# Kernel tuning notes

Measured on AMD Instinct MI355X. Metric: run time of the kernel, lower is better.

The kernel has to match this reference:

```python
import jax, jax.numpy as jnp
import numpy as np
import math
from jax import lax

# cfg['MODEL'] constants
MU = 0.1          # FISTA step size
LMBD = 0.1        # LAMBDA[0], sparsity weight
N_DICT = 1        # EXPANSION_FACTOR
N_STEPS = 6       # NUM_LAYERS (FISTA iterations)
K = 3             # kernel_size
PAD = 1           # padding
STRIDE = 1        # stride (POOLING=False, stride passed to conv)
DN = ('NCHW', 'OIHW', 'NCHW')


def _conv(x, w):
    # F.conv2d(x, w, stride=1, padding=PAD)
    return lax.conv_general_dilated(x, w, (STRIDE, STRIDE), [(PAD, PAD), (PAD, PAD)], dimension_numbers=DN)


def _conv_t(y, w):
    # F.conv_transpose2d(y, w, stride=1, padding=PAD) == conv2d with flipped, in/out-swapped kernel, pad K-1-PAD
    wt = jnp.transpose(jnp.flip(w, (-1, -2)), (1, 0, 2, 3))  # [Cin, Cout, K, K]
    p = K - 1 - PAD
    return lax.conv_general_dilated(y, wt, (1, 1), [(p, p), (p, p)], dimension_numbers=DN)


def _shrink(z, thr):
    # non_negative=True soft-threshold: relu(z - thr)
    return jax.nn.relu(z - thr)


def setup_inputs() -> dict:
    key = jax.random.key(0)
    k1, k2 = jax.random.split(key)
    x = jax.random.normal(k1, (16, 64, 56, 56), dtype=jnp.float32)
    # dictionary weight [out_channels, in_channels*n_dict, K, K], kaiming-ish scale
    W = jax.random.normal(k2, (128, 64 * N_DICT, K, K), dtype=jnp.float32) * 0.05
    return {"x": x, "W": W}


def reference(x, W):
    # w_norm: each output filter normalized to unit Frobenius norm
    Wn = W / jnp.sqrt(jnp.sum(W * W, axis=(1, 2, 3), keepdims=True) + 1e-12)
    thr = MU * LMBD
    xr = jnp.tile(x, (1, N_DICT, 1, 1)) if N_DICT > 1 else x

    # FISTA iteration 0: c = shrink(mu * D^T x)
    c = _shrink(MU * _conv(xr, Wn), thr)
    y = c
    c_prev = c
    t = 1.0
    for _ in range(N_STEPS - 1):
        r = xr - _conv_t(y, Wn)                       # residual x - D c
        c_new = _shrink(y + MU * _conv(r, Wn), thr)   # gradient step + shrink
        t_next = (1.0 + math.sqrt(1.0 + 4.0 * t * t)) / 2.0
        y = c_new + ((t - 1.0) / t_next) * (c_new - c_prev)  # momentum
        c_prev = c_new
        t = t_next
    # POOLING=False -> DictConv2d returns the sparse code directly
    return c_prev
```

## Files before the change

### kernel.cpp

```cpp
#include <hip/hip_runtime.h>
#include <hip/hip_bf16.h>
#include <math.h>

typedef __attribute__((ext_vector_type(8))) short short8;
typedef __attribute__((ext_vector_type(4))) float f32x4;

#define MU_  0.1f
#define THR_ 0.01f
#define ZB_  204

static __device__ inline short f2bf(float f) {
    __hip_bfloat16 h = __float2bfloat16(f);
    return *reinterpret_cast<short*>(&h);
}
static __device__ inline float bf2f(unsigned short u) {
    unsigned int x = ((unsigned int)u) << 16;
    return __builtin_bit_cast(float, x);
}

__global__ __launch_bounds__(256) void prep_kernel(
    const float* __restrict__ x, const float* __restrict__ W,
    short* __restrict__ Rp, short* __restrict__ Yp,
    short* __restrict__ Xp, short* __restrict__ Wf2, short* __restrict__ Wt2) {
    __shared__ float lx[64 * 57];
    const int bid = blockIdx.x, tid = threadIdx.x;
    if (bid < ZB_) {
        int gid = bid * 256 + tid;
        const short8 z = {0, 0, 0, 0, 0, 0, 0, 0};
        if (gid < 17408) {
            int ridx = gid / 544, off = gid - ridx * 544;
            int n = ridx >> 1, row = (ridx & 1) * 57;
            ((short8*)(Rp + ((size_t)(n * 58 + row) * 68) * 64))[off] = z;
        } else {
            int g2 = gid - 17408;
            int ridx = g2 / 1088, off = g2 - ridx * 1088;
            int n = ridx >> 1, row = (ridx & 1) * 57;
            ((short8*)(Yp + ((size_t)(n * 58 + row) * 68) * 128))[off] = z;
        }
    } else if (bid < ZB_ + 32) {
        int co = (bid - ZB_) * 4 + (tid >> 6);
        int ci = tid & 63;
        const float* wp = W + (co * 64 + ci) * 9;
        float v[9]; float s = 0.f;
#pragma unroll
        for (int t = 0; t < 9; ++t) { v[t] = wp[t]; s += v[t] * v[t]; }
#pragma unroll
        for (int off = 32; off; off >>= 1) s += __shfl_xor(s, off, 64);
        float inv = 1.0f / sqrtf(s + 1e-12f);
#pragma unroll
        for (int t = 0; t < 9; ++t) {
            Wf2[((t * 8 + (ci >> 3)) * 128 + co) * 8 + (ci & 7)] = f2bf(v[t] * inv);
            Wt2[((t * 16 + (co >> 3)) * 64 + ci) * 8 + (co & 7)] = f2bf(v[8 - t] * inv);
        }
    } else {
        int pb = bid - ZB_ - 32;
        int row = pb % 58, n = pb / 58;
        short* dst = Xp + ((size_t)(n * 58 + row) * 68) * 64;
        if (row >= 1 && row <= 56) {
            int h = row - 1;
            for (int j = tid; j < 64 * 56; j += 256) {
                int ci = j / 56, w = j - ci * 56;
                lx[ci * 57 + w] = x[((size_t)(n * 64 + ci)) * 3136 + h * 56 + w];
            }
            __syncthreads();
            for (int j = tid; j < 68 * 64; j += 256) {
                int s = j >> 6, ci = j & 63;
                float val = (s >= 2 && s < 58) ? lx[ci * 57 + (s - 2)] : 0.f;
                dst[(s << 6) + (ci ^ ((s & 7) << 3))] = f2bf(val);
            }
        } else {
            for (int j = tid; j < 68 * 64; j += 256) dst[j] = 0;
        }
    }
}

static __device__ __forceinline__ void zero_lds_pads(short* smem, int tid) {
    const short8 z = {0, 0, 0, 0, 0, 0, 0, 0};
    for (int i = tid; i < 288; i += 256) {
        int sr = i >> 3, w = i & 7;
        int row = sr / 12, sl = sr - row * 12;
        int s = (sl < 2) ? sl : sl + 56;
        *(short8*)(smem + (row * 68 + s) * 72 + w * 8) = z;
    }
}

__global__ __launch_bounds__(256, 4) void conv_fwd(
    const short* __restrict__ inp,
    const short* __restrict__ Wf2,
    short* __restrict__ Yp,
    short* __restrict__ Cp,
    float* __restrict__ outp, int mode, float beta) {
    __shared__ __align__(16) short smem[14688];
    const int bid = blockIdx.x, tid = threadIdx.x;
    const int sid = (bid & 7) * 112 + (bid >> 3);
    const int n = sid / 56, r = sid - n * 56 + 1;
    zero_lds_pads(smem, tid);
    {
        const short8* src = (const short8*)(inp + ((size_t)(n * 58 + (r - 1)) * 68) * 64);
        for (int j = tid; j < 1344; j += 256) {
            int sr = j >> 3, w = j & 7;
            int row = sr / 56, s = sr - row * 56 + 2;
            *(short8*)(smem + (row * 68 + s) * 72 + w * 8) = src[(row * 68 + s) * 8 + w];
        }
    }
    const int lane = tid & 63, ct = tid >> 6, quad = lane >> 4, l15 = lane & 15;
    const int cog = ct & 1, pxg = ct >> 1;
    const size_t prow = ((size_t)(n * 58 + r) * 68) * 128;

    short8 yold8[2], cold8[2];
    int pvv[2], pg[2]; bool pok[2];
#pragma unroll
    for (int k = 0; k < 2; ++k) {
        int item = tid + k * 256;
        pok[k] = item < 448;
        pvv[k] = item >> 3; pg[k] = item & 7;
        if (mode != 0 && pok[k]) {
            int s = pvv[k] + 2;
            size_t off = prow + (size_t)s * 128 + 8 * (pg[k] ^ (s & 7));
            yold8[k] = *(const short8*)(Yp + off);
            if (mode == 1) cold8[k] = *(const short8*)(Cp + off);
        }
    }
    __syncthreads();

    f32x4 acc[2][4];
#pragma unroll
    for (int pt = 0; pt < 2; ++pt)
#pragma unroll
        for (int cot = 0; cot < 4; ++cot) acc[pt][cot] = (f32x4){0.f, 0.f, 0.f, 0.f};

#pragma unroll
    for (int f = 0; f < 18; ++f) {
        const int t = f >> 1, half = f & 1;
        const int dh = t / 3, dw = t % 3;
        const int u = l15 + dw + 1;
        const int phys = (half * 4 + quad) ^ (u & 7);
        short8 areg[4];
#pragma unroll
        for (int cot = 0; cot < 4; ++cot) {
            const int co = cog * 64 + cot * 16 + l15;
            areg[cot] = *(const short8*)(Wf2 +
                ((size_t)((t * 8 + half * 4 + quad) * 128 + co)) * 8);
        }
#pragma unroll
        for (int pt = 0; pt < 2; ++pt) {
            const int pti = pxg * 2 + pt;
            const short8 bv = *(const short8*)(smem +
                (dh * 68 + pti * 16 + u) * 72 + phys * 8);
#pragma unroll
            for (int cot = 0; cot < 4; ++cot)
                acc[pt][cot] = __builtin_amdgcn_mfma_f32_16x16x32_bf16(areg[cot], bv, acc[pt][cot], 0, 0, 0);
        }
    }

    __syncthreads();
    short* tb_y = smem;
    short* tb_c = smem + 4608;
    const int h = r - 1;
#pragma unroll
    for (int hh = 0; hh < 2; ++hh) {
        if (mode != 0) {
#pragma unroll
            for (int k = 0; k < 2; ++k) if (pok[k]) {
                int o = pvv[k] * 72 + 8 * (pg[k] ^ (pvv[k] & 3));
                *(short8*)(tb_y + o) = yold8[k];
                if (mode == 1) *(short8*)(tb_c + o) = cold8[k];
            }
        }
        __syncthreads();
        if (hh == 0 && mode != 0) {
#pragma unroll
            for (int k = 0; k < 2; ++k) if (pok[k]) {
                int s = pvv[k] + 2;
                size_t off = prow + (size_t)s * 128 + 8 * ((pg[k] + 8) ^ (s & 7));
                yold8[k] = *(const short8*)(Yp + off);
                if (mode == 1) cold8[k] = *(const short8*)(Cp + off);
            }
        }
        if (cog == hh) {
#pragma unroll
            for (int pt = 0; pt < 2; ++pt) {
                const int px = pxg * 32 + pt * 16 + l15;
#pragma unroll
                for (int cot = 0; cot < 4; ++cot) {
#pragma unroll
                    for (int reg = 0; reg < 4; ++reg) {
                        const int lch = cot * 16 + quad * 4 + reg;
                        const int slot = px * 72 + (lch ^ ((px & 3) << 3));
                        const float a = acc[pt][cot][reg];
                        if (mode == 0) {
                            float c = fmaxf(MU_ * a - THR_, 0.f);
                            short cb16 = f2bf(c);
                            tb_y[slot] = cb16;
                            tb_c[slot] = cb16;
                        } else if (mode == 1) {
                            float yold = bf2f((unsigned short)tb_y[slot]);
                            float cold = bf2f((unsigned short)tb_c[slot]);
                            float c = fmaxf(yold + MU_ * a - THR_, 0.f);
                            tb_y[slot] = f2bf(c + beta * (c - cold));
                            tb_c[slot] = f2bf(c);
                        } else {
                            if (px < 56) {
                                float yold = bf2f((unsigned short)tb_y[slot]);
                                float c = fmaxf(yold + MU_ * a - THR_, 0.f);
                                outp[((size_t)(n * 128 + hh * 64 + lch)) * 3136 + h * 56 + px] = c;
                            }
                        }
                    }
                }
            }
        }
        if (mode != 2) {
            __syncthreads();
            for (int item = tid; item < 448; item += 256) {
                int vv = item >> 3, g = item & 7;
                int so = vv * 72 + 8 * (g ^ (vv & 3));
                short8 yv = *(const short8*)(tb_y + so);
                short8 cv = *(const short8*)(tb_c + so);
                int s = vv + 2;
                size_t off = prow + (size_t)s * 128 + 8 * ((g + 8 * hh) ^ (s & 7));
                *(short8*)(Yp + off) = yv;
                *(short8*)(Cp + off) = cv;
            }
        }
        if (hh == 0) __syncthreads();
    }
}

__global__ __launch_bounds__(256, 4) void conv_t(
    const short* __restrict__ Ypb,
    const short* __restrict__ Wt2,
    const short* __restrict__ Xp,
    short* __restrict__ Rp) {
    __shared__ __align__(16) short smem[14688];
    const int bid = blockIdx.x, tid = threadIdx.x;
    const int sid = (bid & 7) * 112 + (bid >> 3);
    const int n = sid / 56, r = sid - n * 56 + 1;
    const int lane = tid & 63, ct = tid >> 6, quad = lane >> 4, l15 = lane & 15;
    const short8* src = (const short8*)(Ypb + ((size_t)(n * 58 + (r - 1)) * 68) * 128);
    const size_t prow = ((size_t)(n * 58 + r) * 68) * 64;

    short8 xold8[2];
    int pvv[2], pg[2]; bool pok[2];
#pragma unroll
    for (int k = 0; k < 2; ++k) {
        int item = tid + k * 256;
        pok[k] = item < 448;
        pvv[k] = item >> 3; pg[k] = item & 7;
        if (pok[k]) {
            int s = pvv[k] + 2;
            xold8[k] = *(const short8*)(Xp + prow + (size_t)s * 64 + 8 * (pg[k] ^ (s & 7)));
        }
    }

    zero_lds_pads(smem, tid);
    for (int j = tid; j < 1344; j += 256) {
        int sr = j >> 3, w = j & 7;
        int row = sr / 56, s = sr - row * 56 + 2;
        *(short8*)(smem + (row * 68 + s) * 72 + w * 8) = src[(row * 68 + s) * 16 + w];
    }

    f32x4 acc[4];
#pragma unroll
    for (int cit = 0; cit < 4; ++cit) acc[cit] = (f32x4){0.f, 0.f, 0.f, 0.f};

    __syncthreads();

    short8 pf[6];
#pragma unroll
    for (int k = 0; k < 6; ++k) {
        int j = tid + k * 256;
        if (j < 1344) {
            int sr = j >> 3, w = j & 7;
            int row = sr / 56, s = sr - row * 56 + 2;
            pf[k] = src[(row * 68 + s) * 16 + 8 + w];
        }
    }

#pragma unroll
    for (int p = 0; p < 2; ++p) {
        if (p) {
            __syncthreads();
#pragma unroll
            for (int k = 0; k < 6; ++k) {
                int j = tid + k * 256;
                if (j < 1344) {
                    int sr = j >> 3, w = j & 7;
                    int row = sr / 56, s = sr - row * 56 + 2;
                    *(short8*)(smem + (row * 68 + s) * 72 + w * 8) = pf[k];
                }
            }
            __syncthreads();
        }
#pragma unroll
        for (int f = 0; f < 18; ++f) {
            const int t = f >> 1, sh = f & 1;
            const int dh = t / 3, dw = t % 3;
            const int u = l15 + dw + 1;
            const int phys = (sh * 4 + quad) ^ (u & 7);
            short8 areg[4];
#pragma unroll
            for (int cit = 0; cit < 4; ++cit) {
                const int ci = cit * 16 + l15;
                areg[cit] = *(const short8*)(Wt2 +
                    ((size_t)((t * 16 + (p * 2 + sh) * 4 + quad) * 64 + ci)) * 8);
            }
            const short8 bv = *(const short8*)(smem +
                (dh * 68 + ct * 16 + u) * 72 + phys * 8);
#pragma unroll
            for (int cit = 0; cit < 4; ++cit)
                acc[cit] = __builtin_amdgcn_mfma_f32_16x16x32_bf16(areg[cit], bv, acc[cit], 0, 0, 0);
        }
    }

    __syncthreads();
    short* tb = smem;
#pragma unroll
    for (int k = 0; k < 2; ++k) if (pok[k]) {
        *(short8*)(tb + pvv[k] * 72 + 8 * (pg[k] ^ (pvv[k] & 3))) = xold8[k];
    }
    __syncthreads();
    {
        const int px = ct * 16 + l15;
#pragma unroll
        for (int cit = 0; cit < 4; ++cit) {
#pragma unroll
            for (int reg = 0; reg < 4; ++reg) {
                const int cir = cit * 16 + quad * 4 + reg;
                const int slot = px * 72 + (cir ^ ((px & 3) << 3));
                float xo = bf2f((unsigned short)tb[slot]);
                tb[slot] = f2bf(xo - acc[cit][reg]);
            }
        }
    }
    __syncthreads();
    for (int item = tid; item < 448; item += 256) {
        int vv = item >> 3, g = item & 7;
        short8 val = *(const short8*)(tb + vv * 72 + 8 * (g ^ (vv & 3)));
        int s = vv + 2;
        *(short8*)(Rp + prow + (size_t)s * 64 + 8 * (g ^ (s & 7))) = val;
    }
}

extern "C" void kernel_launch(void* const* d_in, const int* in_sizes, int n_in,
                              void* d_out, int out_size, void* d_ws, size_t ws_size,
                              hipStream_t stream) {
    const float* x = (const float*)d_in[0];
    const float* W = (const float*)d_in[1];
    float* out = (float*)d_out;

    const size_t XPN = (size_t)16 * 58 * 68 * 64;
    const size_t YPN = 2 * XPN;
    short* Xp = (short*)d_ws;
    short* Rp = Xp + XPN;
    short* Yp = Rp + XPN;
    short* Cp = Yp + YPN;
    short* Wf2 = Cp + YPN;
    short* Wt2 = Wf2 + 73728;

    const int prep_blocks = ZB_ + 32 + 58 * 16;
    hipLaunchKernelGGL(prep_kernel, dim3(prep_blocks), dim3(256), 0, stream,
                       x, W, Rp, Yp, Xp, Wf2, Wt2);

    dim3 b(256, 1, 1);
    hipLaunchKernelGGL(conv_fwd, dim3(896), b, 0, stream, Xp, Wf2, Yp, Cp,
                       (float*)nullptr, 0, 0.f);
    double t = 1.0;
    for (int it = 1; it <= 5; ++it) {
        hipLaunchKernelGGL(conv_t, dim3(896), b, 0, stream, Yp, Wt2, Xp, Rp);
        double tn = (1.0 + sqrt(1.0 + 4.0 * t * t)) / 2.0;
        float beta = (float)((t - 1.0) / tn);
        hipLaunchKernelGGL(conv_fwd, dim3(896), b, 0, stream, Rp, Wf2, Yp, Cp,
                           (it == 5) ? out : (float*)nullptr, (it == 5) ? 2 : 1,
                           beta);
        t = tn;
    }
}
```

Before: 352.2 us.

## Process two output rows per block in both conv kernels to reuse weights

Each block of conv_fwd and conv_t now computes two adjacent output rows instead of one. It loads four input rows into LDS and reuses each weight A-fragment across both rows, which halves the grid to 448 blocks. The goal is to cut weight loads and halo re-reads per output. In exchange, LDS and accumulator registers roughly double, launch bounds drop to 2 blocks per CU, and the grid of 448 blocks on 256 CUs leaves some CUs with uneven work.

Result: faster. 344.3 us (median of 2 runs) (-2.2%).

```diff
diff --git a/kernel.cpp b/kernel.cpp
--- a/kernel.cpp
+++ b/kernel.cpp
@@ -74,9 +74,9 @@
     }
 }
 
-static __device__ __forceinline__ void zero_lds_pads(short* smem, int tid) {
+static __device__ __forceinline__ void zero_lds_pads4(short* smem, int tid) {
     const short8 z = {0, 0, 0, 0, 0, 0, 0, 0};
-    for (int i = tid; i < 288; i += 256) {
+    for (int i = tid; i < 384; i += 256) {
         int sr = i >> 3, w = i & 7;
         int row = sr / 12, sl = sr - row * 12;
         int s = (sl < 2) ? sl : sl + 56;
@@ -84,20 +84,20 @@
     }
 }
 
-__global__ __launch_bounds__(256, 4) void conv_fwd(
+__global__ __launch_bounds__(256, 2) void conv_fwd(
     const short* __restrict__ inp,
     const short* __restrict__ Wf2,
     short* __restrict__ Yp,
     short* __restrict__ Cp,
     float* __restrict__ outp, int mode, float beta) {
-    __shared__ __align__(16) short smem[14688];
+    __shared__ __align__(16) short smem[38016];
     const int bid = blockIdx.x, tid = threadIdx.x;
-    const int sid = (bid & 7) * 112 + (bid >> 3);
-    const int n = sid / 56, r = sid - n * 56 + 1;
-    zero_lds_pads(smem, tid);
+    const int sid0 = (bid & 7) * 112 + (bid >> 3) * 2;
+    const int n = sid0 / 56, r0 = sid0 - n * 56 + 1;
+    zero_lds_pads4(smem, tid);
     {
-        const short8* src = (const short8*)(inp + ((size_t)(n * 58 + (r - 1)) * 68) * 64);
-        for (int j = tid; j < 1344; j += 256) {
+        const short8* src = (const short8*)(inp + ((size_t)(n * 58 + (r0 - 1)) * 68) * 64);
+        for (int j = tid; j < 1792; j += 256) {
             int sr = j >> 3, w = j & 7;
             int row = sr / 56, s = sr - row * 56 + 2;
             *(short8*)(smem + (row * 68 + s) * 72 + w * 8) = src[(row * 68 + s) * 8 + w];
@@ -105,9 +105,11 @@
     }
     const int lane = tid & 63, ct = tid >> 6, quad = lane >> 4, l15 = lane & 15;
     const int cog = ct & 1, pxg = ct >> 1;
-    const size_t prow = ((size_t)(n * 58 + r) * 68) * 128;
-
-    short8 yold8[2], cold8[2];
+    size_t prow[2];
+    prow[0] = ((size_t)(n * 58 + r0) * 68) * 128;
+    prow[1] = prow[0] + 68 * 128;
+
+    short8 yold8[2][2], cold8[2][2];
     int pvv[2], pg[2]; bool pok[2];
 #pragma unroll
     for (int k = 0; k < 2; ++k) {
@@ -116,18 +118,24 @@
         pvv[k] = item >> 3; pg[k] = item & 7;
         if (mode != 0 && pok[k]) {
             int s = pvv[k] + 2;
-            size_t off = prow + (size_t)s * 128 + 8 * (pg[k] ^ (s & 7));
-            yold8[k] = *(const short8*)(Yp + off);
-            if (mode == 1) cold8[k] = *(const short8*)(Cp + off);
+            int xo = 8 * (pg[k] ^ (s & 7));
+#pragma unroll
+            for (int rw = 0; rw < 2; ++rw) {
+                size_t off = prow[rw] + (size_t)s * 128 + xo;
+                yold8[rw][k] = *(const short8*)(Yp + off);
+                if (mode == 1) cold8[rw][k] = *(const short8*)(Cp + off);
+            }
         }
     }
     __syncthreads();
 
-    f32x4 acc[2][4];
-#pragma unroll
-    for (int pt = 0; pt < 2; ++pt)
-#pragma unroll
-        for (int cot = 0; cot < 4; ++cot) acc[pt][cot] = (f32x4){0.f, 0.f, 0.f, 0.f};
+    f32x4 acc[2][2][4];
+#pragma unroll
+    for (int rw = 0; rw < 2; ++rw)
+#pragma unroll
+        for (int pt = 0; pt < 2; ++pt)
+#pragma unroll
+            for (int cot = 0; cot < 4; ++cot) acc[rw][pt][cot] = (f32x4){0.f, 0.f, 0.f, 0.f};
 
 #pragma unroll
     for (int f = 0; f < 18; ++f) {
@@ -143,28 +151,34 @@
                 ((size_t)((t * 8 + half * 4 + quad) * 128 + co)) * 8);
         }
 #pragma unroll
-        for (int pt = 0; pt < 2; ++pt) {
-            const int pti = pxg * 2 + pt;
-            const short8 bv = *(const short8*)(smem +
-                (dh * 68 + pti * 16 + u) * 72 + phys * 8);
-#pragma unroll
-            for (int cot = 0; cot < 4; ++cot)
-                acc[pt][cot] = __builtin_amdgcn_mfma_f32_16x16x32_bf16(areg[cot], bv, acc[pt][cot], 0, 0, 0);
-        }
-    }
-
-    __syncthreads();
-    short* tb_y = smem;
-    short* tb_c = smem + 4608;
-    const int h = r - 1;
+        for (int rw = 0; rw < 2; ++rw) {
+#pragma unroll
+            for (int pt = 0; pt < 2; ++pt) {
+                const int pti = pxg * 2 + pt;
+                const short8 bv = *(const short8*)(smem +
+                    ((dh + rw) * 68 + pti * 16 + u) * 72 + phys * 8);
+#pragma unroll
+                for (int cot = 0; cot < 4; ++cot)
+                    acc[rw][pt][cot] = __builtin_amdgcn_mfma_f32_16x16x32_bf16(areg[cot], bv, acc[rw][pt][cot], 0, 0, 0);
+            }
+        }
+    }
+
+    short* tbase = smem + 19584;
+    const int h0 = r0 - 1;
 #pragma unroll
     for (int hh = 0; hh < 2; ++hh) {
         if (mode != 0) {
 #pragma unroll
-            for (int k = 0; k < 2; ++k) if (pok[k]) {
-                int o = pvv[k] * 72 + 8 * (pg[k] ^ (pvv[k] & 3));
-                *(short8*)(tb_y + o) = yold8[k];
-                if (mode == 1) *(short8*)(tb_c + o) = cold8[k];
+            for (int rw = 0; rw < 2; ++rw) {
+                short* tb_y = tbase + rw * 9216;
+                short* tb_c = tb_y + 4608;
+#pragma unroll
+                for (int k = 0; k < 2; ++k) if (pok[k]) {
+                    int o = pvv[k] * 72 + 8 * (pg[k] ^ (pvv[k] & 3));
+                    *(short8*)(tb_y + o) = yold8[rw][k];
+                    if (mode == 1) *(short8*)(tb_c + o) = cold8[rw][k];
+                }
             }
         }
         __syncthreads();
@@ -172,38 +186,47 @@
 #pragma unroll
             for (int k = 0; k < 2; ++k) if (pok[k]) {
                 int s = pvv[k] + 2;
-                size_t off = prow + (size_t)s * 128 + 8 * ((pg[k] + 8) ^ (s & 7));
-                yold8[k] = *(const short8*)(Yp + off);
-                if (mode == 1) cold8[k] = *(const short8*)(Cp + off);
+                int xo = 8 * ((pg[k] + 8) ^ (s & 7));
+#pragma unroll
+                for (int rw = 0; rw < 2; ++rw) {
+                    size_t off = prow[rw] + (size_t)s * 128 + xo;
+                    yold8[rw][k] = *(const short8*)(Yp + off);
+                    if (mode == 1) cold8[rw][k] = *(const short8*)(Cp + off);
+                }
             }
         }
         if (cog == hh) {
 #pragma unroll
-            for (int pt = 0; pt < 2; ++pt) {
-                const int px = pxg * 32 + pt * 16 + l15;
-#pragma unroll
-                for (int cot = 0; cot < 4; ++cot) {
-#pragma unroll
-                    for (int reg = 0; reg < 4; ++reg) {
-                        const int lch = cot * 16 + quad * 4 + reg;
-                        const int slot = px * 72 + (lch ^ ((px & 3) << 3));
-                        const float a = acc[pt][cot][reg];
-                        if (mode == 0) {
-                            float c = fmaxf(MU_ * a - THR_, 0.f);
-                            short cb16 = f2bf(c);
-                            tb_y[slot] = cb16;
-                            tb_c[slot] = cb16;
-                        } else if (mode == 1) {
-                            float yold = bf2f((unsigned short)tb_y[slot]);
-                            float cold = bf2f((unsigned short)tb_c[slot]);
-                            float c = fmaxf(yold + MU_ * a - THR_, 0.f);
-                            tb_y[slot] = f2bf(c + beta * (c - cold));
-                            tb_c[slot] = f2bf(c);
-                        } else {
-                            if (px < 56) {
+            for (int rw = 0; rw < 2; ++rw) {
+                short* tb_y = tbase + rw * 9216;
+                short* tb_c = tb_y + 4608;
+#pragma unroll
+                for (int pt = 0; pt < 2; ++pt) {
+                    const int px = pxg * 32 + pt * 16 + l15;
+#pragma unroll
+                    for (int cot = 0; cot < 4; ++cot) {
+#pragma unroll
+                        for (int reg = 0; reg < 4; ++reg) {
+                            const int lch = cot * 16 + quad * 4 + reg;
+                            const int slot = px * 72 + (lch ^ ((px & 3) << 3));
+                            const float a = acc[rw][pt][cot][reg];
+                            if (mode == 0) {
+                                float c = fmaxf(MU_ * a - THR_, 0.f);
+                                short cb16 = f2bf(c);
+                                tb_y[slot] = cb16;
+                                tb_c[slot] = cb16;
+                            } else if (mode == 1) {
                                 float yold = bf2f((unsigned short)tb_y[slot]);
+                                float cold = bf2f((unsigned short)tb_c[slot]);
                                 float c = fmaxf(yold + MU_ * a - THR_, 0.f);
-                                outp[((size_t)(n * 128 + hh * 64 + lch)) * 3136 + h * 56 + px] = c;
+                                tb_y[slot] = f2bf(c + beta * (c - cold));
+                                tb_c[slot] = f2bf(c);
+                            } else {
+                                if (px < 56) {
+                                    float yold = bf2f((unsigned short)tb_y[slot]);
+                                    float c = fmaxf(yold + MU_ * a - THR_, 0.f);
+                                    outp[((size_t)(n * 128 + hh * 64 + lch)) * 3136 + (h0 + rw) * 56 + px] = c;
+                                }
                             }
                         }
                     }
@@ -215,32 +238,39 @@
             for (int item = tid; item < 448; item += 256) {
                 int vv = item >> 3, g = item & 7;
                 int so = vv * 72 + 8 * (g ^ (vv & 3));
-                short8 yv = *(const short8*)(tb_y + so);
-                short8 cv = *(const short8*)(tb_c + so);
                 int s = vv + 2;
-                size_t off = prow + (size_t)s * 128 + 8 * ((g + 8 * hh) ^ (s & 7));
-                *(short8*)(Yp + off) = yv;
-                *(short8*)(Cp + off) = cv;
+                int xo = 8 * ((g + 8 * hh) ^ (s & 7));
+#pragma unroll
+                for (int rw = 0; rw < 2; ++rw) {
+                    short* tb_y = tbase + rw * 9216;
+                    short8 yv = *(const short8*)(tb_y + so);
+                    short8 cv = *(const short8*)(tb_y + 4608 + so);
+                    size_t off = prow[rw] + (size_t)s * 128 + xo;
+                    *(short8*)(Yp + off) = yv;
+                    *(short8*)(Cp + off) = cv;
+                }
             }
         }
         if (hh == 0) __syncthreads();
     }
 }
 
-__global__ __launch_bounds__(256, 4) void conv_t(
+__global__ __launch_bounds__(256, 2) void conv_t(
     const short* __restrict__ Ypb,
     const short* __restrict__ Wt2,
     const short* __restrict__ Xp,
     short* __restrict__ Rp) {
-    __shared__ __align__(16) short smem[14688];
+    __shared__ __align__(16) short smem[28800];
     const int bid = blockIdx.x, tid = threadIdx.x;
-    const int sid = (bid & 7) * 112 + (bid >> 3);
-    const int n = sid / 56, r = sid - n * 56 + 1;
+    const int sid0 = (bid & 7) * 112 + (bid >> 3) * 2;
+    const int n = sid0 / 56, r0 = sid0 - n * 56 + 1;
     const int lane = tid & 63, ct = tid >> 6, quad = lane >> 4, l15 = lane & 15;
-    const short8* src = (const short8*)(Ypb + ((size_t)(n * 58 + (r - 1)) * 68) * 128);
-    const size_t prow = ((size_t)(n * 58 + r) * 68) * 64;
-
-    short8 xold8[2];
+    const short8* src = (const short8*)(Ypb + ((size_t)(n * 58 + (r0 - 1)) * 68) * 128);
+    size_t prowX[2];
+    prowX[0] = ((size_t)(n * 58 + r0) * 68) * 64;
+    prowX[1] = prowX[0] + 68 * 64;
+
+    short8 xold8[2][2];
     int pvv[2], pg[2]; bool pok[2];
 #pragma unroll
     for (int k = 0; k < 2; ++k) {
@@ -249,28 +279,33 @@
         pvv[k] = item >> 3; pg[k] = item & 7;
         if (pok[k]) {
             int s = pvv[k] + 2;
-            xold8[k] = *(const short8*)(Xp + prow + (size_t)s * 64 + 8 * (pg[k] ^ (s & 7)));
-        }
-    }
-
-    zero_lds_pads(smem, tid);
-    for (int j = tid; j < 1344; j += 256) {
+            int xo = 8 * (pg[k] ^ (s & 7));
+#pragma unroll
+            for (int rw = 0; rw < 2; ++rw)
+                xold8[rw][k] = *(const short8*)(Xp + prowX[rw] + (size_t)s * 64 + xo);
+        }
+    }
+
+    zero_lds_pads4(smem, tid);
+    for (int j = tid; j < 1792; j += 256) {
         int sr = j >> 3, w = j & 7;
         int row = sr / 56, s = sr - row * 56 + 2;
         *(short8*)(smem + (row * 68 + s) * 72 + w * 8) = src[(row * 68 + s) * 16 + w];
     }
 
-    f32x4 acc[4];
-#pragma unroll
-    for (int cit = 0; cit < 4; ++cit) acc[cit] = (f32x4){0.f, 0.f, 0.f, 0.f};
+    f32x4 acc[2][4];
+#pragma unroll
+    for (int rw = 0; rw < 2; ++rw)
+#pragma unroll
+        for (int cit = 0; cit < 4; ++cit) acc[rw][cit] = (f32x4){0.f, 0.f, 0.f, 0.f};
 
     __syncthreads();
 
-    short8 pf[6];
-#pragma unroll
-    for (int k = 0; k < 6; ++k) {
+    short8 pf[7];
+#pragma unroll
+    for (int k = 0; k < 7; ++k) {
         int j = tid + k * 256;
-        if (j < 1344) {
+        if (j < 1792) {
             int sr = j >> 3, w = j & 7;
             int row = sr / 56, s = sr - row * 56 + 2;
             pf[k] = src[(row * 68 + s) * 16 + 8 + w];
@@ -282,9 +317,9 @@
         if (p) {
             __syncthreads();
 #pragma unroll
-            for (int k = 0; k < 6; ++k) {
+            for (int k = 0; k < 7; ++k) {
                 int j = tid + k * 256;
-                if (j < 1344) {
+                if (j < 1792) {
                     int sr = j >> 3, w = j & 7;
                     int row = sr / 56, s = sr - row * 56 + 2;
                     *(short8*)(smem + (row * 68 + s) * 72 + w * 8) = pf[k];
@@ -305,40 +340,54 @@
                 areg[cit] = *(const short8*)(Wt2 +
                     ((size_t)((t * 16 + (p * 2 + sh) * 4 + quad) * 64 + ci)) * 8);
             }
-            const short8 bv = *(const short8*)(smem +
-                (dh * 68 + ct * 16 + u) * 72 + phys * 8);
-#pragma unroll
-            for (int cit = 0; cit < 4; ++cit)
-                acc[cit] = __builtin_amdgcn_mfma_f32_16x16x32_bf16(areg[cit], bv, acc[cit], 0, 0, 0);
-        }
-    }
-
-    __syncthreads();
-    short* tb = smem;
-#pragma unroll
-    for (int k = 0; k < 2; ++k) if (pok[k]) {
-        *(short8*)(tb + pvv[k] * 72 + 8 * (pg[k] ^ (pvv[k] & 3))) = xold8[k];
+#pragma unroll
+            for (int rw = 0; rw < 2; ++rw) {
+                const short8 bv = *(const short8*)(smem +
+                    ((dh + rw) * 68 + ct * 16 + u) * 72 + phys * 8);
+#pragma unroll
+                for (int cit = 0; cit < 4; ++cit)
+                    acc[rw][cit] = __builtin_amdgcn_mfma_f32_16x16x32_bf16(areg[cit], bv, acc[rw][cit], 0, 0, 0);
+            }
+        }
+    }
+
+    short* tbase = smem + 19584;
+#pragma unroll
+    for (int rw = 0; rw < 2; ++rw) {
+#pragma unroll
+        for (int k = 0; k < 2; ++k) if (pok[k]) {
+            *(short8*)(tbase + rw * 4608 + pvv[k] * 72 + 8 * (pg[k] ^ (pvv[k] & 3))) = xold8[rw][k];
+        }
     }
     __syncthreads();
     {
         const int px = ct * 16 + l15;
 #pragma unroll
-        for (int cit = 0; cit < 4; ++cit) {
-#pragma unroll
-            for (int reg = 0; reg < 4; ++reg) {
-                const int cir = cit * 16 + quad * 4 + reg;
-                const int slot = px * 72 + (cir ^ ((px & 3) << 3));
-                float xo = bf2f((unsigned short)tb[slot]);
-                tb[slot] = f2bf(xo - acc[cit][reg]);
+        for (int rw = 0; rw < 2; ++rw) {
+            short* tb = tbase + rw * 4608;
+#pragma unroll
+            for (int cit = 0; cit < 4; ++cit) {
+#pragma unroll
+                for (int reg = 0; reg < 4; ++reg) {
+                    const int cir = cit * 16 + quad * 4 + reg;
+                    const int slot = px * 72 + (cir ^ ((px & 3) << 3));
+                    float xo = bf2f((unsigned short)tb[slot]);
+                    tb[slot] = f2bf(xo - acc[rw][cit][reg]);
+                }
             }
         }
     }
     __syncthreads();
     for (int item = tid; item < 448; item += 256) {
         int vv = item >> 3, g = item & 7;
-        short8 val = *(const short8*)(tb + vv * 72 + 8 * (g ^ (vv & 3)));
+        int so = vv * 72 + 8 * (g ^ (vv & 3));
         int s = vv + 2;
-        *(short8*)(Rp + prow + (size_t)s * 64 + 8 * (g ^ (s & 7))) = val;
+        int xo = 8 * (g ^ (s & 7));
+#pragma unroll
+        for (int rw = 0; rw < 2; ++rw) {
+            short8 val = *(const short8*)(tbase + rw * 4608 + so);
+            *(short8*)(Rp + prowX[rw] + (size_t)s * 64 + xo) = val;
+        }
     }
 }
 
@@ -363,14 +412,14 @@
                        x, W, Rp, Yp, Xp, Wf2, Wt2);
 
     dim3 b(256, 1, 1);
-    hipLaunchKernelGGL(conv_fwd, dim3(896), b, 0, stream, Xp, Wf2, Yp, Cp,
+    hipLaunchKernelGGL(conv_fwd, dim3(448), b, 0, stream, Xp, Wf2, Yp, Cp,
                        (float*)nullptr, 0, 0.f);
     double t = 1.0;
     for (int it = 1; it <= 5; ++it) {
-        hipLaunchKernelGGL(conv_t, dim3(896), b, 0, stream, Yp, Wt2, Xp, Rp);
+        hipLaunchKernelGGL(conv_t, dim3(448), b, 0, stream, Yp, Wt2, Xp, Rp);
         double tn = (1.0 + sqrt(1.0 + 4.0 * t * t)) / 2.0;
         float beta = (float)((t - 1.0) / tn);
-        hipLaunchKernelGGL(conv_fwd, dim3(896), b, 0, stream, Rp, Wf2, Yp, Cp,
+        hipLaunchKernelGGL(conv_fwd, dim3(448), b, 0, stream, Rp, Wf2, Yp, Cp,
                            (it == 5) ? out : (float*)nullptr, (it == 5) ? 2 : 1,
                            beta);
         t = tn;
```
